# Performance work log

Measured on AMD Instinct MI355X. Metric: run time of the kernel, lower is better.

Reference implementation:

```python
import jax, jax.numpy as jnp
import numpy as np

# MoE config (matches init_kwargs)
T = 16384   # tokens
H = 1024    # hidden size
I = 1024    # intermediate size per expert
E = 8       # n_experts
TOPK = 2
RENORMALIZE = True


def setup_inputs() -> dict:
    key = jax.random.key(0)
    ks = jax.random.split(key, 6)
    x = jax.random.normal(ks[0], (T, H), dtype=jnp.float32)
    gating_output = jax.random.normal(ks[1], (T, E), dtype=jnp.float32)
    # fp8-quantized weights simulated as their integer-grid values in fp32;
    # dequant = q * per-expert scalar scale (normalize_e4m3fn_to_native_float8 path)
    w1 = jax.random.normal(ks[2], (E, 2 * I, H), dtype=jnp.float32)  # fused [gate; up]
    w2 = jax.random.normal(ks[3], (E, H, I), dtype=jnp.float32)      # down_proj
    w1_scale = jax.random.uniform(ks[4], (E,), dtype=jnp.float32, minval=0.01, maxval=0.05)
    w2_scale = jax.random.uniform(ks[5], (E,), dtype=jnp.float32, minval=0.01, maxval=0.05)
    return {"x": x, "gating_output": gating_output, "w1": w1, "w2": w2,
            "w1_scale": w1_scale, "w2_scale": w2_scale}


def _moe(x, gating_output, w1, w2, w1_scale, w2_scale):
    # softmax scoring -> top-k routing (use_grouped_topk=False)
    probs = jax.nn.softmax(gating_output, axis=-1)              # [T, E]
    topk_w, topk_idx = jax.lax.top_k(probs, TOPK)               # [T, K]
    if RENORMALIZE:
        topk_w = topk_w / jnp.sum(topk_w, axis=-1, keepdims=True)
    out = jnp.zeros_like(x)
    for e in range(E):  # fixed small expert count: grouped-GEMM reference
        w1e = w1[e] * w1_scale[e]                               # dequant [2I, H]
        w2e = w2[e] * w2_scale[e]                               # dequant [H, I]
        gate = x @ w1e[:I].T                                    # [T, I]
        up = x @ w1e[I:].T                                      # [T, I]
        h = jax.nn.silu(gate) * up                              # SwiGLU
        y = h @ w2e.T                                           # [T, H]
        # per-token routing weight for this expert (0 if not routed)
        coef = jnp.sum(jnp.where(topk_idx == e, topk_w, 0.0), axis=-1)  # [T]
        out = out + coef[:, None] * y
    return out


def reference(x, gating_output, w1, w2, w1_scale, w2_scale):
    return _moe(x, gating_output, w1, w2, w1_scale, w2_scale)
```

## Files before the change

kernel.cpp:

```cpp
#include <hip/hip_runtime.h>
#include <hip/hip_bf16.h>

#define T_TOK 16384
#define H_DIM 1024
#define I_DIM 1024
#define E_NUM 8
#define NPAIR (T_TOK * 2)
#define BM 128
#define BM2 64
#define BK 64
#define MAX_MT (NPAIR / BM + E_NUM)
#define MAX_MT2 (NPAIR / BM2 + E_NUM)

typedef float v4f __attribute__((ext_vector_type(4)));
typedef float v16f __attribute__((ext_vector_type(16)));
typedef short v8s __attribute__((ext_vector_type(8)));

__device__ __forceinline__ unsigned short f2bf(float f) {
    unsigned int u = __float_as_uint(f);
    unsigned int r = (u + 0x7fffu + ((u >> 16) & 1u)) >> 16;
    return (unsigned short)r;
}
__device__ __forceinline__ float bf2f(unsigned short s) {
    return __uint_as_float(((unsigned int)s) << 16);
}

__device__ __forceinline__ void gl_lds16(const void* g, void* l) {
    __builtin_amdgcn_global_load_lds(
        (const __attribute__((address_space(1))) void*)g,
        (__attribute__((address_space(3))) void*)l, 16, 0, 0);
}

__device__ __forceinline__ int swz(int row, int unit) {
    return row * 64 + ((unit ^ (row & 7)) << 3);
}

__global__ void k_route(const float* __restrict__ gating,
                        int* __restrict__ tokExp, float* __restrict__ tokW,
                        int* __restrict__ counts) {
    int t = blockIdx.x * 256 + threadIdx.x;
    int lane = threadIdx.x & 63;
    float g[E_NUM];
#pragma unroll
    for (int e = 0; e < E_NUM; e++) g[e] = gating[t * E_NUM + e];
    int i0 = 0; float v0 = g[0];
#pragma unroll
    for (int e = 1; e < E_NUM; e++) if (g[e] > v0) { v0 = g[e]; i0 = e; }
    int i1 = -1; float v1 = -1e30f;
#pragma unroll
    for (int e = 0; e < E_NUM; e++) if (e != i0 && g[e] > v1) { v1 = g[e]; i1 = e; }
    float w0 = 1.f / (1.f + __expf(v1 - v0));
    tokExp[2 * t] = i0; tokExp[2 * t + 1] = i1;
    tokW[2 * t] = w0;   tokW[2 * t + 1] = 1.f - w0;
#pragma unroll
    for (int e = 0; e < E_NUM; e++) {
        unsigned long long mA = __ballot(i0 == e);
        unsigned long long mB = __ballot(i1 == e);
        int c = __popcll(mA) + __popcll(mB);
        if (lane == 0 && c) atomicAdd(&counts[e], c);
    }
}

__global__ void k_scan(const int* __restrict__ counts, int* __restrict__ offsets,
                       int* __restrict__ tileOff, int* __restrict__ tileOff2,
                       int* __restrict__ cursor) {
    if (threadIdx.x == 0 && blockIdx.x == 0) {
        int o = 0, to = 0, to2 = 0;
        for (int e = 0; e < E_NUM; e++) {
            offsets[e] = o; tileOff[e] = to; tileOff2[e] = to2; cursor[e] = o;
            o += counts[e];
            to += (counts[e] + BM - 1) / BM;
            to2 += (counts[e] + BM2 - 1) / BM2;
        }
        offsets[E_NUM] = o; tileOff[E_NUM] = to; tileOff2[E_NUM] = to2;
    }
}

__global__ void k_scatter(const int* __restrict__ tokExp, const float* __restrict__ tokW,
                          int* __restrict__ cursor,
                          int* __restrict__ pairTok, float* __restrict__ pairW,
                          int* __restrict__ invMap) {
    int t = blockIdx.x * 256 + threadIdx.x;
    int lane = threadIdx.x & 63;
#pragma unroll
    for (int k = 0; k < 2; k++) {
        int e = tokExp[2 * t + k];
        int pos = 0;
#pragma unroll
        for (int ex = 0; ex < E_NUM; ex++) {
            unsigned long long m = __ballot(e == ex);
            if (m) {
                int leader = __builtin_ctzll(m);
                int base = 0;
                if (lane == leader) base = atomicAdd(&cursor[ex], __popcll(m));
                base = __shfl(base, leader);
                if (e == ex) pos = base + __popcll(m & ((1ull << lane) - 1ull));
            }
        }
        pairTok[pos] = t;
        pairW[pos] = tokW[2 * t + k];
        invMap[2 * t + k] = pos;
    }
}

__global__ void k_cvt_x(const float* __restrict__ src, unsigned short* __restrict__ dst) {
    size_t i4 = ((size_t)blockIdx.x * 256 + threadIdx.x) * 4;
    float4 v = *(const float4*)(src + i4);
    ushort4 o;
    o.x = f2bf(v.x); o.y = f2bf(v.y); o.z = f2bf(v.z); o.w = f2bf(v.w);
    *(ushort4*)(dst + i4) = o;
}

__global__ void k_cvt_w(const float* __restrict__ src, unsigned short* __restrict__ dst,
                        const float* __restrict__ scale, int shift) {
    size_t i4 = ((size_t)blockIdx.x * 256 + threadIdx.x) * 4;
    float s = scale[i4 >> shift];
    float4 v = *(const float4*)(src + i4);
    ushort4 o;
    o.x = f2bf(v.x * s); o.y = f2bf(v.y * s); o.z = f2bf(v.z * s); o.w = f2bf(v.w * s);
    *(ushort4*)(dst + i4) = o;
}

__global__ __launch_bounds__(256, 3)
void k_gemm1(const unsigned short* __restrict__ xbf,
             const unsigned short* __restrict__ w1bf,
             const int* __restrict__ pairTok,
             const int* __restrict__ offsets, const int* __restrict__ tileOff,
             unsigned short* __restrict__ hbuf) {
    __shared__ unsigned short lA[BM * BK];
    __shared__ unsigned short lB[BM * BK];

    int mt = blockIdx.x;
    if (mt >= tileOff[E_NUM]) return;
    int e = 0;
    while (mt >= tileOff[e + 1]) e++;
    int row0 = offsets[e] + (mt - tileOff[e]) * BM;
    int valid = offsets[e + 1] - row0; if (valid > BM) valid = BM;

    int nt = blockIdx.y;
    int tid = threadIdx.x;
    int lane = tid & 63, wave = tid >> 6;
    int wm = wave & 1, role = wave >> 1;

    int lr = lane >> 3;
    int lcs = ((lane & 7) ^ lr) * 8;

    const unsigned short* wg = w1bf + (size_t)e * 2 * I_DIM * H_DIM + (size_t)(nt * 64) * H_DIM;
    const unsigned short* wu = wg + (size_t)I_DIM * H_DIM;
    const unsigned short* bsrc = (wave & 2) ? wu : wg;

    int tokRow[4];
#pragma unroll
    for (int j = 0; j < 4; j++) {
        int r = wave * 32 + j * 8 + lr;
        int rc = r < valid ? r : valid - 1;
        tokRow[j] = pairTok[row0 + rc];
    }

    v16f acc[2][2];
#pragma unroll
    for (int i = 0; i < 2; i++)
#pragma unroll
        for (int j = 0; j < 2; j++) acc[i][j] = (v16f)0.f;

    for (int ko = 0; ko < H_DIM / BK; ko++) {
        int k0 = ko * BK;
        __syncthreads();
#pragma unroll
        for (int j = 0; j < 4; j++)
            gl_lds16(xbf + (size_t)tokRow[j] * H_DIM + k0 + lcs, lA + (wave * 4 + j) * 512);
#pragma unroll
        for (int j = 0; j < 4; j++) {
            int srcrow = (wave & 1) * 32 + j * 8 + lr;
            gl_lds16(bsrc + (size_t)srcrow * H_DIM + k0 + lcs, lB + (wave * 4 + j) * 512);
        }
        __syncthreads();
#pragma unroll
        for (int kk = 0; kk < BK; kk += 16) {
            int u = (kk >> 3) + (lane >> 5);
            v8s a[2], b[2];
#pragma unroll
            for (int i = 0; i < 2; i++)
                a[i] = *(const v8s*)(lA + swz(wm * 64 + i * 32 + (lane & 31), u));
#pragma unroll
            for (int j = 0; j < 2; j++)
                b[j] = *(const v8s*)(lB + swz(role * 64 + j * 32 + (lane & 31), u));
#pragma unroll
            for (int i = 0; i < 2; i++)
#pragma unroll
                for (int j = 0; j < 2; j++)
                    acc[i][j] = __builtin_amdgcn_mfma_f32_32x32x16_bf16(a[i], b[j], acc[i][j], 0, 0, 0);
        }
    }

    int half = lane >> 5, c = lane & 31;
    __syncthreads();
    if (role == 1) {
#pragma unroll
        for (int i = 0; i < 2; i++)
#pragma unroll
            for (int r = 0; r < 16; r++) {
                int row = wm * 64 + i * 32 + (r & 3) + 8 * (r >> 2) + 4 * half;
#pragma unroll
                for (int j = 0; j < 2; j++)
                    lB[row * 64 + j * 32 + c] = f2bf(acc[i][j][r]);
            }
    }
    __syncthreads();
    if (role == 0) {
#pragma unroll
        for (int i = 0; i < 2; i++)
#pragma unroll
            for (int r = 0; r < 16; r++) {
                int row = wm * 64 + i * 32 + (r & 3) + 8 * (r >> 2) + 4 * half;
                if (row < valid) {
                    size_t base = (size_t)(row0 + row) * I_DIM + nt * 64;
#pragma unroll
                    for (int j = 0; j < 2; j++) {
                        float g = acc[i][j][r];
                        float uu = bf2f(lB[row * 64 + j * 32 + c]);
                        float s = g / (1.f + __expf(-g));
                        hbuf[base + j * 32 + c] = f2bf(s * uu);
                    }
                }
            }
    }
}

__global__ __launch_bounds__(256, 3)
void k_gemm2(const unsigned short* __restrict__ hbuf,
             const unsigned short* __restrict__ w2bf,
             const float* __restrict__ pairW,
             const int* __restrict__ offsets, const int* __restrict__ tileOff2,
             unsigned short* __restrict__ ybuf) {
    __shared__ unsigned short lA[BM2 * BK];
    __shared__ unsigned short lB[256 * BK];

    int mt = blockIdx.x;
    if (mt >= tileOff2[E_NUM]) return;
    int e = 0;
    while (mt >= tileOff2[e + 1]) e++;
    int row0 = offsets[e] + (mt - tileOff2[e]) * BM2;
    int valid = offsets[e + 1] - row0; if (valid > BM2) valid = BM2;

    int nt = blockIdx.y;
    int tid = threadIdx.x;
    int lane = tid & 63, wave = tid >> 6;
    int wm = wave & 1, wn = wave >> 1;

    int lr = lane >> 3;
    int lcs = ((lane & 7) ^ lr) * 8;

    const unsigned short* w2e = w2bf + (size_t)e * H_DIM * I_DIM + (size_t)(nt * 256) * I_DIM;

    int rowA[2];
#pragma unroll
    for (int j = 0; j < 2; j++) {
        int r = wave * 16 + j * 8 + lr;
        int rc = r < valid ? r : valid - 1;
        rowA[j] = row0 + rc;
    }

    v16f acc[4];
#pragma unroll
    for (int j = 0; j < 4; j++) acc[j] = (v16f)0.f;

    for (int ko = 0; ko < I_DIM / BK; ko++) {
        int k0 = ko * BK;
        __syncthreads();
#pragma unroll
        for (int j = 0; j < 2; j++)
            gl_lds16(hbuf + (size_t)rowA[j] * I_DIM + k0 + lcs, lA + (wave * 2 + j) * 512);
#pragma unroll
        for (int j = 0; j < 8; j++)
            gl_lds16(w2e + (size_t)(wave * 64 + j * 8 + lr) * I_DIM + k0 + lcs,
                     lB + (wave * 8 + j) * 512);
        __syncthreads();
#pragma unroll
        for (int kk = 0; kk < BK; kk += 16) {
            int u = (kk >> 3) + (lane >> 5);
            v8s a = *(const v8s*)(lA + swz(wm * 32 + (lane & 31), u));
            v8s b[4];
#pragma unroll
            for (int j = 0; j < 4; j++)
                b[j] = *(const v8s*)(lB + swz(wn * 128 + j * 32 + (lane & 31), u));
#pragma unroll
            for (int j = 0; j < 4; j++)
                acc[j] = __builtin_amdgcn_mfma_f32_32x32x16_bf16(a, b[j], acc[j], 0, 0, 0);
        }
    }

    int half = lane >> 5, c = lane & 31;
#pragma unroll
    for (int r = 0; r < 16; r++) {
        int row = wm * 32 + (r & 3) + 8 * (r >> 2) + 4 * half;
        if (row < valid) {
            int pos = row0 + row;
            float coef = pairW[pos];
            unsigned short* orow = ybuf + (size_t)pos * H_DIM + nt * 256 + wn * 128;
#pragma unroll
            for (int j = 0; j < 4; j++)
                orow[j * 32 + c] = f2bf(coef * acc[j][r]);
        }
    }
}

__global__ __launch_bounds__(256)
void k_reduce(const unsigned short* __restrict__ ybuf,
              const int* __restrict__ invMap,
              float* __restrict__ out) {
    int t = blockIdx.x;
    int p0 = invMap[2 * t], p1 = invMap[2 * t + 1];
    int c4 = threadIdx.x * 4;
    ushort4 a = *(const ushort4*)(ybuf + (size_t)p0 * H_DIM + c4);
    ushort4 b = *(const ushort4*)(ybuf + (size_t)p1 * H_DIM + c4);
    float4 o;
    o.x = bf2f(a.x) + bf2f(b.x);
    o.y = bf2f(a.y) + bf2f(b.y);
    o.z = bf2f(a.z) + bf2f(b.z);
    o.w = bf2f(a.w) + bf2f(b.w);
    *(float4*)(out + (size_t)t * H_DIM + c4) = o;
}

extern "C" void kernel_launch(void* const* d_in, const int* in_sizes, int n_in,
                              void* d_out, int out_size, void* d_ws, size_t ws_size,
                              hipStream_t stream) {
    const float* x      = (const float*)d_in[0];
    const float* gating = (const float*)d_in[1];
    const float* w1     = (const float*)d_in[2];
    const float* w2     = (const float*)d_in[3];
    const float* w1s    = (const float*)d_in[4];
    const float* w2s    = (const float*)d_in[5];
    float* out = (float*)d_out;

    char* ws = (char*)d_ws;
    size_t off = 0;
    auto alloc = [&](size_t bytes) { void* p = ws + off; off += (bytes + 255) & ~(size_t)255; return p; };
    unsigned short* xbf  = (unsigned short*)alloc((size_t)T_TOK * H_DIM * 2);
    unsigned short* w1bf = (unsigned short*)alloc((size_t)E_NUM * 2 * I_DIM * H_DIM * 2);
    unsigned short* w2bf = (unsigned short*)alloc((size_t)E_NUM * H_DIM * I_DIM * 2);
    unsigned short* hbuf = (unsigned short*)alloc((size_t)NPAIR * I_DIM * 2);
    unsigned short* ybuf = (unsigned short*)alloc((size_t)NPAIR * H_DIM * 2);
    int*   pairTok  = (int*)alloc(NPAIR * 4);
    float* pairW    = (float*)alloc(NPAIR * 4);
    int*   tokExp   = (int*)alloc(NPAIR * 4);
    float* tokW     = (float*)alloc(NPAIR * 4);
    int*   invMap   = (int*)alloc(NPAIR * 4);
    int*   counts   = (int*)alloc(64);
    int*   offsets  = (int*)alloc(64);
    int*   tileOff  = (int*)alloc(64);
    int*   tileOff2 = (int*)alloc(64);
    int*   cursor   = (int*)alloc(64);

    hipMemsetAsync(counts, 0, 64, stream);

    k_route<<<T_TOK / 256, 256, 0, stream>>>(gating, tokExp, tokW, counts);
    k_scan<<<1, 64, 0, stream>>>(counts, offsets, tileOff, tileOff2, cursor);
    k_scatter<<<T_TOK / 256, 256, 0, stream>>>(tokExp, tokW, cursor, pairTok, pairW, invMap);
    k_cvt_x<<<(T_TOK * H_DIM / 4) / 256, 256, 0, stream>>>(x, xbf);
    k_cvt_w<<<(E_NUM * 2 * I_DIM * H_DIM / 4) / 256, 256, 0, stream>>>(w1, w1bf, w1s, 21);
    k_cvt_w<<<(E_NUM * H_DIM * I_DIM / 4) / 256, 256, 0, stream>>>(w2, w2bf, w2s, 20);

    dim3 g1(MAX_MT, I_DIM / 64);
    k_gemm1<<<g1, 256, 0, stream>>>(xbf, w1bf, pairTok, offsets, tileOff, hbuf);
    dim3 g2(MAX_MT2, H_DIM / 256);
    k_gemm2<<<g2, 256, 0, stream>>>(hbuf, w2bf, pairW, offsets, tileOff2, ybuf);
    k_reduce<<<T_TOK, 256, 0, stream>>>(ybuf, invMap, out);
}
```

Measured before the change: 580.6 us.

## Enlarge both MoE GEMM tiles to 512-thread blocks with wider N/M tiles

GEMM1 now uses 512 threads with a 128-row by 128-column tile covering both the gate and up halves, doubling the N width per block. GEMM2 moves from a 64-row to a 128-row M tile with 8 waves arranged 2x4, sharing the same tile offsets as GEMM1. Larger tiles raise arithmetic intensity and reuse of the A and B tiles in LDS, cutting global loads per MFMA. In exchange, LDS use per block grows and blocks are larger, which may lower occupancy and waste more work on partially filled expert tail tiles.

Result: faster. 561.1 us (-3.4%).

```diff
diff --git a/kernel.cpp b/kernel.cpp
--- a/kernel.cpp
+++ b/kernel.cpp
@@ -7,10 +7,8 @@
 #define E_NUM 8
 #define NPAIR (T_TOK * 2)
 #define BM 128
-#define BM2 64
 #define BK 64
 #define MAX_MT (NPAIR / BM + E_NUM)
-#define MAX_MT2 (NPAIR / BM2 + E_NUM)
 
 typedef float v4f __attribute__((ext_vector_type(4)));
 typedef float v16f __attribute__((ext_vector_type(16)));
@@ -62,17 +60,15 @@
 }
 
 __global__ void k_scan(const int* __restrict__ counts, int* __restrict__ offsets,
-                       int* __restrict__ tileOff, int* __restrict__ tileOff2,
-                       int* __restrict__ cursor) {
+                       int* __restrict__ tileOff, int* __restrict__ cursor) {
     if (threadIdx.x == 0 && blockIdx.x == 0) {
-        int o = 0, to = 0, to2 = 0;
+        int o = 0, to = 0;
         for (int e = 0; e < E_NUM; e++) {
-            offsets[e] = o; tileOff[e] = to; tileOff2[e] = to2; cursor[e] = o;
+            offsets[e] = o; tileOff[e] = to; cursor[e] = o;
             o += counts[e];
             to += (counts[e] + BM - 1) / BM;
-            to2 += (counts[e] + BM2 - 1) / BM2;
-        }
-        offsets[E_NUM] = o; tileOff[E_NUM] = to; tileOff2[E_NUM] = to2;
+        }
+        offsets[E_NUM] = o; tileOff[E_NUM] = to;
     }
 }
 
@@ -121,14 +117,14 @@
     *(ushort4*)(dst + i4) = o;
 }
 
-__global__ __launch_bounds__(256, 3)
+__global__ __launch_bounds__(512, 4)
 void k_gemm1(const unsigned short* __restrict__ xbf,
              const unsigned short* __restrict__ w1bf,
              const int* __restrict__ pairTok,
              const int* __restrict__ offsets, const int* __restrict__ tileOff,
              unsigned short* __restrict__ hbuf) {
     __shared__ unsigned short lA[BM * BK];
-    __shared__ unsigned short lB[BM * BK];
+    __shared__ unsigned short lB[256 * BK];
 
     int mt = blockIdx.x;
     if (mt >= tileOff[E_NUM]) return;
@@ -140,21 +136,28 @@
     int nt = blockIdx.y;
     int tid = threadIdx.x;
     int lane = tid & 63, wave = tid >> 6;
-    int wm = wave & 1, role = wave >> 1;
+    int role = wave >> 2, quad = wave & 3;
+    int wm = quad >> 1, wn = quad & 1;
 
     int lr = lane >> 3;
     int lcs = ((lane & 7) ^ lr) * 8;
 
-    const unsigned short* wg = w1bf + (size_t)e * 2 * I_DIM * H_DIM + (size_t)(nt * 64) * H_DIM;
+    const unsigned short* wg = w1bf + (size_t)e * 2 * I_DIM * H_DIM + (size_t)(nt * 128) * H_DIM;
     const unsigned short* wu = wg + (size_t)I_DIM * H_DIM;
-    const unsigned short* bsrc = (wave & 2) ? wu : wg;
-
-    int tokRow[4];
-#pragma unroll
-    for (int j = 0; j < 4; j++) {
-        int r = wave * 32 + j * 8 + lr;
+
+    int tokRow[2];
+#pragma unroll
+    for (int j = 0; j < 2; j++) {
+        int r = wave * 16 + j * 8 + lr;
         int rc = r < valid ? r : valid - 1;
         tokRow[j] = pairTok[row0 + rc];
+    }
+    const unsigned short* bRow[4];
+#pragma unroll
+    for (int j = 0; j < 4; j++) {
+        int brow = wave * 32 + j * 8 + lr;
+        bRow[j] = (brow < 128) ? (wg + (size_t)brow * H_DIM)
+                               : (wu + (size_t)(brow - 128) * H_DIM);
     }
 
     v16f acc[2][2];
@@ -167,13 +170,11 @@
         int k0 = ko * BK;
         __syncthreads();
 #pragma unroll
+        for (int j = 0; j < 2; j++)
+            gl_lds16(xbf + (size_t)tokRow[j] * H_DIM + k0 + lcs, lA + (wave * 2 + j) * 512);
+#pragma unroll
         for (int j = 0; j < 4; j++)
-            gl_lds16(xbf + (size_t)tokRow[j] * H_DIM + k0 + lcs, lA + (wave * 4 + j) * 512);
-#pragma unroll
-        for (int j = 0; j < 4; j++) {
-            int srcrow = (wave & 1) * 32 + j * 8 + lr;
-            gl_lds16(bsrc + (size_t)srcrow * H_DIM + k0 + lcs, lB + (wave * 4 + j) * 512);
-        }
+            gl_lds16(bRow[j] + k0 + lcs, lB + (wave * 4 + j) * 512);
         __syncthreads();
 #pragma unroll
         for (int kk = 0; kk < BK; kk += 16) {
@@ -184,7 +185,7 @@
                 a[i] = *(const v8s*)(lA + swz(wm * 64 + i * 32 + (lane & 31), u));
 #pragma unroll
             for (int j = 0; j < 2; j++)
-                b[j] = *(const v8s*)(lB + swz(role * 64 + j * 32 + (lane & 31), u));
+                b[j] = *(const v8s*)(lB + swz(role * 128 + wn * 64 + j * 32 + (lane & 31), u));
 #pragma unroll
             for (int i = 0; i < 2; i++)
 #pragma unroll
@@ -203,7 +204,7 @@
                 int row = wm * 64 + i * 32 + (r & 3) + 8 * (r >> 2) + 4 * half;
 #pragma unroll
                 for (int j = 0; j < 2; j++)
-                    lB[row * 64 + j * 32 + c] = f2bf(acc[i][j][r]);
+                    lB[row * 128 + wn * 64 + j * 32 + c] = f2bf(acc[i][j][r]);
             }
     }
     __syncthreads();
@@ -214,39 +215,39 @@
             for (int r = 0; r < 16; r++) {
                 int row = wm * 64 + i * 32 + (r & 3) + 8 * (r >> 2) + 4 * half;
                 if (row < valid) {
-                    size_t base = (size_t)(row0 + row) * I_DIM + nt * 64;
+                    size_t base = (size_t)(row0 + row) * I_DIM + nt * 128;
 #pragma unroll
                     for (int j = 0; j < 2; j++) {
                         float g = acc[i][j][r];
-                        float uu = bf2f(lB[row * 64 + j * 32 + c]);
+                        float uu = bf2f(lB[row * 128 + wn * 64 + j * 32 + c]);
                         float s = g / (1.f + __expf(-g));
-                        hbuf[base + j * 32 + c] = f2bf(s * uu);
+                        hbuf[base + wn * 64 + j * 32 + c] = f2bf(s * uu);
                     }
                 }
             }
     }
 }
 
-__global__ __launch_bounds__(256, 3)
+__global__ __launch_bounds__(512, 4)
 void k_gemm2(const unsigned short* __restrict__ hbuf,
              const unsigned short* __restrict__ w2bf,
              const float* __restrict__ pairW,
-             const int* __restrict__ offsets, const int* __restrict__ tileOff2,
+             const int* __restrict__ offsets, const int* __restrict__ tileOff,
              unsigned short* __restrict__ ybuf) {
-    __shared__ unsigned short lA[BM2 * BK];
+    __shared__ unsigned short lA[BM * BK];
     __shared__ unsigned short lB[256 * BK];
 
     int mt = blockIdx.x;
-    if (mt >= tileOff2[E_NUM]) return;
+    if (mt >= tileOff[E_NUM]) return;
     int e = 0;
-    while (mt >= tileOff2[e + 1]) e++;
-    int row0 = offsets[e] + (mt - tileOff2[e]) * BM2;
-    int valid = offsets[e + 1] - row0; if (valid > BM2) valid = BM2;
+    while (mt >= tileOff[e + 1]) e++;
+    int row0 = offsets[e] + (mt - tileOff[e]) * BM;
+    int valid = offsets[e + 1] - row0; if (valid > BM) valid = BM;
 
     int nt = blockIdx.y;
     int tid = threadIdx.x;
     int lane = tid & 63, wave = tid >> 6;
-    int wm = wave & 1, wn = wave >> 1;
+    int wm = wave >> 2, wn = wave & 3;
 
     int lr = lane >> 3;
     int lcs = ((lane & 7) ^ lr) * 8;
@@ -261,9 +262,11 @@
         rowA[j] = row0 + rc;
     }
 
-    v16f acc[4];
-#pragma unroll
-    for (int j = 0; j < 4; j++) acc[j] = (v16f)0.f;
+    v16f acc[2][2];
+#pragma unroll
+    for (int i = 0; i < 2; i++)
+#pragma unroll
+        for (int j = 0; j < 2; j++) acc[i][j] = (v16f)0.f;
 
     for (int ko = 0; ko < I_DIM / BK; ko++) {
         int k0 = ko * BK;
@@ -272,37 +275,43 @@
         for (int j = 0; j < 2; j++)
             gl_lds16(hbuf + (size_t)rowA[j] * I_DIM + k0 + lcs, lA + (wave * 2 + j) * 512);
 #pragma unroll
-        for (int j = 0; j < 8; j++)
-            gl_lds16(w2e + (size_t)(wave * 64 + j * 8 + lr) * I_DIM + k0 + lcs,
-                     lB + (wave * 8 + j) * 512);
+        for (int j = 0; j < 4; j++)
+            gl_lds16(w2e + (size_t)(wave * 32 + j * 8 + lr) * I_DIM + k0 + lcs,
+                     lB + (wave * 4 + j) * 512);
         __syncthreads();
 #pragma unroll
         for (int kk = 0; kk < BK; kk += 16) {
             int u = (kk >> 3) + (lane >> 5);
-            v8s a = *(const v8s*)(lA + swz(wm * 32 + (lane & 31), u));
-            v8s b[4];
-#pragma unroll
-            for (int j = 0; j < 4; j++)
-                b[j] = *(const v8s*)(lB + swz(wn * 128 + j * 32 + (lane & 31), u));
-#pragma unroll
-            for (int j = 0; j < 4; j++)
-                acc[j] = __builtin_amdgcn_mfma_f32_32x32x16_bf16(a, b[j], acc[j], 0, 0, 0);
+            v8s a[2], b[2];
+#pragma unroll
+            for (int i = 0; i < 2; i++)
+                a[i] = *(const v8s*)(lA + swz(wm * 64 + i * 32 + (lane & 31), u));
+#pragma unroll
+            for (int j = 0; j < 2; j++)
+                b[j] = *(const v8s*)(lB + swz(wn * 64 + j * 32 + (lane & 31), u));
+#pragma unroll
+            for (int i = 0; i < 2; i++)
+#pragma unroll
+                for (int j = 0; j < 2; j++)
+                    acc[i][j] = __builtin_amdgcn_mfma_f32_32x32x16_bf16(a[i], b[j], acc[i][j], 0, 0, 0);
         }
     }
 
     int half = lane >> 5, c = lane & 31;
 #pragma unroll
-    for (int r = 0; r < 16; r++) {
-        int row = wm * 32 + (r & 3) + 8 * (r >> 2) + 4 * half;
-        if (row < valid) {
-            int pos = row0 + row;
-            float coef = pairW[pos];
-            unsigned short* orow = ybuf + (size_t)pos * H_DIM + nt * 256 + wn * 128;
-#pragma unroll
-            for (int j = 0; j < 4; j++)
-                orow[j * 32 + c] = f2bf(coef * acc[j][r]);
-        }
-    }
+    for (int i = 0; i < 2; i++)
+#pragma unroll
+        for (int r = 0; r < 16; r++) {
+            int row = wm * 64 + i * 32 + (r & 3) + 8 * (r >> 2) + 4 * half;
+            if (row < valid) {
+                int pos = row0 + row;
+                float coef = pairW[pos];
+                unsigned short* orow = ybuf + (size_t)pos * H_DIM + nt * 256;
+#pragma unroll
+                for (int j = 0; j < 2; j++)
+                    orow[wn * 64 + j * 32 + c] = f2bf(coef * acc[i][j][r]);
+            }
+        }
 }
 
 __global__ __launch_bounds__(256)
@@ -349,21 +358,20 @@
     int*   counts   = (int*)alloc(64);
     int*   offsets  = (int*)alloc(64);
     int*   tileOff  = (int*)alloc(64);
-    int*   tileOff2 = (int*)alloc(64);
     int*   cursor   = (int*)alloc(64);
 
     hipMemsetAsync(counts, 0, 64, stream);
 
     k_route<<<T_TOK / 256, 256, 0, stream>>>(gating, tokExp, tokW, counts);
-    k_scan<<<1, 64, 0, stream>>>(counts, offsets, tileOff, tileOff2, cursor);
+    k_scan<<<1, 64, 0, stream>>>(counts, offsets, tileOff, cursor);
     k_scatter<<<T_TOK / 256, 256, 0, stream>>>(tokExp, tokW, cursor, pairTok, pairW, invMap);
     k_cvt_x<<<(T_TOK * H_DIM / 4) / 256, 256, 0, stream>>>(x, xbf);
     k_cvt_w<<<(E_NUM * 2 * I_DIM * H_DIM / 4) / 256, 256, 0, stream>>>(w1, w1bf, w1s, 21);
     k_cvt_w<<<(E_NUM * H_DIM * I_DIM / 4) / 256, 256, 0, stream>>>(w2, w2bf, w2s, 20);
 
-    dim3 g1(MAX_MT, I_DIM / 64);
-    k_gemm1<<<g1, 256, 0, stream>>>(xbf, w1bf, pairTok, offsets, tileOff, hbuf);
-    dim3 g2(MAX_MT2, H_DIM / 256);
-    k_gemm2<<<g2, 256, 0, stream>>>(hbuf, w2bf, pairW, offsets, tileOff2, ybuf);
+    dim3 g1(MAX_MT, I_DIM / 128);
+    k_gemm1<<<g1, 512, 0, stream>>>(xbf, w1bf, pairTok, offsets, tileOff, hbuf);
+    dim3 g2(MAX_MT, H_DIM / 256);
+    k_gemm2<<<g2, 512, 0, stream>>>(hbuf, w2bf, pairW, offsets, tileOff, ybuf);
     k_reduce<<<T_TOK, 256, 0, stream>>>(ybuf, invMap, out);
 }
```
